# Kernel optimization log

Measured on AMD Instinct MI355X. Metric: run time of the kernel, lower is better.

## Reference

```python
import jax, jax.numpy as jnp
import numpy as np

T, B, D, H, NQ = 2048, 512, 128, 128, 8

def setup_inputs() -> dict:
    key = jax.random.key(0)
    ks = jax.random.split(key, 9)
    s = 1.0 / np.sqrt(D + H)
    inp = {"inputs": jax.random.normal(ks[0], (T, B, D), dtype=jnp.float32)}
    names = ["Wf", "bf", "Wi", "bi", "Wu", "bu", "Wo", "bo"]
    for j, nm in enumerate(names):
        shp = (NQ, D + H) if nm.startswith("W") else (NQ,)
        inp[nm] = jax.random.normal(ks[j + 1], shp, dtype=jnp.float32) * s
    return inp


def _qgate(z):
    # Expected fraction of '1' outcomes after RX(theta_i)|0> on each wire:
    # P(1) = sin^2(theta/2); mean over wires -> one scalar per sample.
    # (Deterministic expectation in place of the 100-shot Aer sampling; the
    # appended random_circuit is unseeded/non-deterministic and is omitted.)
    return jnp.mean(jnp.sin(z * 0.5) ** 2, axis=-1)  # [B]


def reference(inputs, Wf, bf, Wi, bi, Wu, bu, Wo, bo):
    Bsz = inputs.shape[1]
    h0 = jnp.zeros((Bsz, H), dtype=inputs.dtype)
    c0 = jnp.zeros((Bsz, H), dtype=inputs.dtype)

    def step(carry, x):
        hx, cx = carry
        comb = jnp.concatenate([x, hx], axis=1)  # [B, D+H]
        f = jax.nn.sigmoid(_qgate(comb @ Wf.T + bf))[:, None]
        i = jax.nn.sigmoid(_qgate(comb @ Wi.T + bi))[:, None]
        g = jnp.tanh(_qgate(comb @ Wu.T + bu))[:, None]
        o = jax.nn.sigmoid(_qgate(comb @ Wo.T + bo))[:, None]
        cx = f * cx + i * g
        hx = o * jnp.tanh(cx)
        return (hx, cx), hx

    (hx, cx), stacked = jax.lax.scan(step, (h0, c0), inputs)
    return stacked, hx, cx
```

## Files before the change

kernel.cpp:

```cpp
#include <hip/hip_runtime.h>
#include <stdint.h>


typedef __attribute__((ext_vector_type(8))) short short8;
typedef __attribute__((ext_vector_type(4))) float float4v;

#define TSTEPS 2048
#define BATCH  512
#define DIMX   128
#define HID    128
#define TBLK   (TSTEPS / 8)
#define LROW   33
#define LBUF   (16 * LROW)

template <int CTRL>
__device__ __forceinline__ float dppf(float x) {
  return __int_as_float(
      __builtin_amdgcn_mov_dpp(__float_as_int(x), CTRL, 0xF, 0xF, true));
}

__device__ __forceinline__ void splitv(float4v a, float4v b,
                                       short8& hi, short8& lo) {
#pragma unroll
  for (int j = 0; j < 8; ++j) {
    float x = (j < 4) ? a[j] : b[j - 4];
    unsigned int u = __float_as_uint(x);
    float r = x - __uint_as_float(u & 0xFFFF0000u);
    hi[j] = (short)(u >> 16);
    lo[j] = (short)(__float_as_uint(r) >> 16);
  }
}

__global__ __launch_bounds__(64) void qlstm_fused(
    const float* __restrict__ X,
    const float* __restrict__ Wf, const float* __restrict__ bfv,
    const float* __restrict__ Wi, const float* __restrict__ biv,
    const float* __restrict__ Wu, const float* __restrict__ buv,
    const float* __restrict__ Wo, const float* __restrict__ bov,
    float* __restrict__ out)
{
  __shared__ float Zl[2 * LBUF];

  const int lane  = threadIdx.x;
  const int m     = lane & 15;
  const int quad  = lane >> 4;
  const int g32   = lane & 31;
  const int gate  = g32 >> 3;
  const int q     = g32 & 7;
  const int bhalf = lane >> 5;
  const int b0    = blockIdx.x * 2;

  const int qm = m & 7;
  const float* Bt0 = (m < 8) ? Wf : Wi;
  const float* Bt1 = (m < 8) ? Wu : Wo;
  short8 b0h[4], b0l[4], b1h[4], b1l[4];
#pragma unroll
  for (int ks = 0; ks < 4; ++ks) {
    const float* p0 = Bt0 + qm * 256 + ks * 32 + quad * 8;
    const float* p1 = Bt1 + qm * 256 + ks * 32 + quad * 8;
    splitv(*(const float4v*)p0, *(const float4v*)(p0 + 4), b0h[ks], b0l[ks]);
    splitv(*(const float4v*)p1, *(const float4v*)(p1 + 4), b1h[ks], b1l[ks]);
  }
  const float INV2PI = 0.15915494309189535f;
  const float bias0 = ((m < 8) ? bfv : biv)[qm];
  const float bias1 = ((m < 8) ? buv : bov)[qm];

  const float* Wsel = (gate == 0) ? Wf : (gate == 1) ? Wi
                    : (gate == 2) ? Wu : Wo;
  const float* wp = Wsel + q * 256 + 128;
  float ws = 0.f;
#pragma unroll 8
  for (int j = 0; j < 128; ++j) ws += wp[j];
  const float wrev = ws * INV2PI;

  const float L2E = 1.4426950408889634f;
  const float ka = (gate == 2) ? (L2E / 8.f) : (L2E / 16.f);
  const float kb = (gate == 2) ? (-L2E)      : (-0.5f * L2E);
  const float s2 = (gate == 2) ? 2.f : 1.f;
  const float s3 = (gate == 2) ? -1.f : 0.f;

  const int base32 = lane & 32;
  const int adr_f = (base32 + 0  + q) * 4;
  const int adr_i = (base32 + 8  + q) * 4;
  const int adr_u = (base32 + 16 + q) * 4;
  const int adr_o = (base32 + 24 + q) * 4;

  const float* arow = X + ((long)(m >> 1) * BATCH + b0 + (m & 1)) * DIMX;
  float4v Aa[8];

#define LOADA(tb)                                                            \
  {                                                                          \
    const float* p_ = arow + (long)(tb) * (8 * BATCH * DIMX);                \
    _Pragma("unroll")                                                        \
    for (int ks_ = 0; ks_ < 4; ++ks_) {                                      \
      Aa[2 * ks_]     = *(const float4v*)(p_ + ks_ * 32 + quad * 8);         \
      Aa[2 * ks_ + 1] = *(const float4v*)(p_ + ks_ * 32 + quad * 8 + 4);     \
    }                                                                        \
  }

#define PRODUCE(buf)                                                         \
  {                                                                          \
    float4v acc0 = {0.f, 0.f, 0.f, 0.f};                                     \
    float4v acc1 = {0.f, 0.f, 0.f, 0.f};                                     \
    _Pragma("unroll")                                                        \
    for (int ks_ = 0; ks_ < 4; ++ks_) {                                      \
      short8 ah_, al_;                                                       \
      splitv(Aa[2 * ks_], Aa[2 * ks_ + 1], ah_, al_);                        \
      acc0 = __builtin_amdgcn_mfma_f32_16x16x32_bf16(ah_, b0h[ks_], acc0, 0, 0, 0); \
      acc0 = __builtin_amdgcn_mfma_f32_16x16x32_bf16(al_, b0h[ks_], acc0, 0, 0, 0); \
      acc0 = __builtin_amdgcn_mfma_f32_16x16x32_bf16(ah_, b0l[ks_], acc0, 0, 0, 0); \
      acc1 = __builtin_amdgcn_mfma_f32_16x16x32_bf16(ah_, b1h[ks_], acc1, 0, 0, 0); \
      acc1 = __builtin_amdgcn_mfma_f32_16x16x32_bf16(al_, b1h[ks_], acc1, 0, 0, 0); \
      acc1 = __builtin_amdgcn_mfma_f32_16x16x32_bf16(ah_, b1l[ks_], acc1, 0, 0, 0); \
    }                                                                        \
    _Pragma("unroll")                                                        \
    for (int r_ = 0; r_ < 4; ++r_) {                                         \
      int row_ = quad * 4 + r_;                                              \
      Zl[(buf) * LBUF + row_ * LROW + m]      = (acc0[r_] + bias0) * INV2PI; \
      Zl[(buf) * LBUF + row_ * LROW + m + 16] = (acc1[r_] + bias1) * INV2PI; \
    }                                                                        \
  }

  float c = 0.f, h = 0.f;
  float* orow = out + (long)(b0 + bhalf) * HID + g32 * 4;

  LOADA(0);
  PRODUCE(0);
  LOADA(1);

  for (int k = 0; k < TBLK; ++k) {
    PRODUCE((k + 1) & 1);
    int kn = k + 2; if (kn > TBLK - 1) kn = TBLK - 1;
    LOADA(kn);

    const float* zb = Zl + (k & 1) * LBUF + bhalf * LROW + g32;
#pragma unroll
    for (int j = 0; j < 8; ++j) {
      float zx = zb[j * 2 * LROW];

      float r  = __builtin_fmaf(h, wrev, zx);
      float cs = __builtin_amdgcn_cosf(r);

      float s = cs + dppf<0x141>(cs);
      s += dppf<0xB1>(s);
      s += dppf<0x4E>(s);

      float e = __builtin_amdgcn_exp2f(__builtin_fmaf(s, ka, kb));
      float v = __builtin_fmaf(__builtin_amdgcn_rcpf(1.f + e), s2, s3);

      float fg = __int_as_float(__builtin_amdgcn_ds_bpermute(adr_f, __float_as_int(v)));
      float ig = __int_as_float(__builtin_amdgcn_ds_bpermute(adr_i, __float_as_int(v)));
      float ug = __int_as_float(__builtin_amdgcn_ds_bpermute(adr_u, __float_as_int(v)));
      float og = __int_as_float(__builtin_amdgcn_ds_bpermute(adr_o, __float_as_int(v)));

      c = __builtin_fmaf(fg, c, ig * ug);
      float e2 = __builtin_amdgcn_exp2f(c * (2.f * L2E));
      float th = __builtin_fmaf(-2.f, __builtin_amdgcn_rcpf(1.f + e2), 1.f);
      h = og * th;

      float4v hv = {h, h, h, h};
      *(float4v*)orow = hv;
      orow += (long)BATCH * HID;
    }
  }

  float4v hv = {h, h, h, h};
  float4v cv = {c, c, c, c};
  float* hxp = out + (long)TSTEPS * BATCH * HID + (long)(b0 + bhalf) * HID + g32 * 4;
  *(float4v*)hxp = hv;
  *(float4v*)(hxp + BATCH * HID) = cv;
#undef LOADA
#undef PRODUCE
}

extern "C" void kernel_launch(void* const* d_in, const int* in_sizes, int n_in,
                              void* d_out, int out_size, void* d_ws, size_t ws_size,
                              hipStream_t stream) {
  (void)in_sizes; (void)n_in; (void)out_size; (void)d_ws; (void)ws_size;
  const float* X   = (const float*)d_in[0];
  const float* Wf  = (const float*)d_in[1];
  const float* bfv = (const float*)d_in[2];
  const float* Wi  = (const float*)d_in[3];
  const float* biv = (const float*)d_in[4];
  const float* Wu  = (const float*)d_in[5];
  const float* buv = (const float*)d_in[6];
  const float* Wo  = (const float*)d_in[7];
  const float* bov = (const float*)d_in[8];
  float* out = (float*)d_out;

  qlstm_fused<<<BATCH / 2, 64, 0, stream>>>(X, Wf, bfv, Wi, biv, Wu, buv, Wo, bov, out);
}
```

Before: 994.6 us.

## Interleave MFMA production with recurrence and remap lanes to cut cross-lane shuffles

The lane layout changes so that each lane handles two qubits of one gate. Gate values are then broadcast within a quad using DPP instead of four ds_bpermute ops, and the qubit reduction drops from three DPP steps to two. The next block's MFMA work and A-load are spread across the eight serial recurrence steps so the matrix unit overlaps the latency-bound gate chain. The recurrence is also reformulated algebraically: c is tracked in scaled exp2 units, h-dependent terms are precomputed from og and rc, and the ug*2-1 step is folded in. This shortens the dependency chain but changes rounding and adds register pressure.

```diff
diff --git a/kernel.cpp b/kernel.cpp
--- a/kernel.cpp
+++ b/kernel.cpp
@@ -45,8 +45,8 @@
   const int m     = lane & 15;
   const int quad  = lane >> 4;
   const int g32   = lane & 31;
-  const int gate  = g32 >> 3;
-  const int q     = g32 & 7;
+  const int gate  = g32 & 3;
+  const int qq    = (g32 >> 2) & 3;
   const int bhalf = lane >> 5;
   const int b0    = blockIdx.x * 2;
 
@@ -67,23 +67,19 @@
 
   const float* Wsel = (gate == 0) ? Wf : (gate == 1) ? Wi
                     : (gate == 2) ? Wu : Wo;
-  const float* wp = Wsel + q * 256 + 128;
-  float ws = 0.f;
+  const float* wpa = Wsel + qq * 256 + 128;
+  const float* wpb = Wsel + (qq + 4) * 256 + 128;
+  float wsa = 0.f, wsb = 0.f;
 #pragma unroll 8
-  for (int j = 0; j < 128; ++j) ws += wp[j];
-  const float wrev = ws * INV2PI;
+  for (int j = 0; j < 128; ++j) { wsa += wpa[j]; wsb += wpb[j]; }
+  const float wrev0 = wsa * INV2PI;
+  const float wrev1 = wsb * INV2PI;
 
   const float L2E = 1.4426950408889634f;
   const float ka = (gate == 2) ? (L2E / 8.f) : (L2E / 16.f);
   const float kb = (gate == 2) ? (-L2E)      : (-0.5f * L2E);
-  const float s2 = (gate == 2) ? 2.f : 1.f;
-  const float s3 = (gate == 2) ? -1.f : 0.f;
-
-  const int base32 = lane & 32;
-  const int adr_f = (base32 + 0  + q) * 4;
-  const int adr_i = (base32 + 8  + q) * 4;
-  const int adr_u = (base32 + 16 + q) * 4;
-  const int adr_o = (base32 + 24 + q) * 4;
+  const int zc0 = gate * 8 + qq;
+  const int zc1 = zc0 + 4;
 
   const float* arow = X + ((long)(m >> 1) * BATCH + b0 + (m & 1)) * DIMX;
   float4v Aa[8];
@@ -121,7 +117,12 @@
     }                                                                        \
   }
 
-  float c = 0.f, h = 0.f;
+  float cc = 0.f;
+  float rc = 0.f;
+  float og = 0.f;
+  float ogw0 = 0.f, ogw1 = 0.f;
+  float n2g0 = 0.f, n2g1 = 0.f;
+  float h = 0.f;
   float* orow = out + (long)(b0 + bhalf) * HID + g32 * 4;
 
   LOADA(0);
@@ -129,34 +130,70 @@
   LOADA(1);
 
   for (int k = 0; k < TBLK; ++k) {
-    PRODUCE((k + 1) & 1);
-    int kn = k + 2; if (kn > TBLK - 1) kn = TBLK - 1;
-    LOADA(kn);
-
-    const float* zb = Zl + (k & 1) * LBUF + bhalf * LROW + g32;
+    const int wbuf = (k + 1) & 1;
+
+    const float* zb = Zl + (k & 1) * LBUF + bhalf * LROW;
+    float zx0[8], zx1[8];
 #pragma unroll
     for (int j = 0; j < 8; ++j) {
-      float zx = zb[j * 2 * LROW];
-
-      float r  = __builtin_fmaf(h, wrev, zx);
-      float cs = __builtin_amdgcn_cosf(r);
-
-      float s = cs + dppf<0x141>(cs);
-      s += dppf<0xB1>(s);
-      s += dppf<0x4E>(s);
-
-      float e = __builtin_amdgcn_exp2f(__builtin_fmaf(s, ka, kb));
-      float v = __builtin_fmaf(__builtin_amdgcn_rcpf(1.f + e), s2, s3);
-
-      float fg = __int_as_float(__builtin_amdgcn_ds_bpermute(adr_f, __float_as_int(v)));
-      float ig = __int_as_float(__builtin_amdgcn_ds_bpermute(adr_i, __float_as_int(v)));
-      float ug = __int_as_float(__builtin_amdgcn_ds_bpermute(adr_u, __float_as_int(v)));
-      float og = __int_as_float(__builtin_amdgcn_ds_bpermute(adr_o, __float_as_int(v)));
-
-      c = __builtin_fmaf(fg, c, ig * ug);
-      float e2 = __builtin_amdgcn_exp2f(c * (2.f * L2E));
-      float th = __builtin_fmaf(-2.f, __builtin_amdgcn_rcpf(1.f + e2), 1.f);
-      h = og * th;
+      zx0[j] = zb[j * 2 * LROW + zc0];
+      zx1[j] = zb[j * 2 * LROW + zc1];
+    }
+
+    float4v acc0 = {0.f, 0.f, 0.f, 0.f};
+    float4v acc1 = {0.f, 0.f, 0.f, 0.f};
+    short8 ah, al;
+
+#pragma unroll
+    for (int j = 0; j < 8; ++j) {
+      {
+        const int ks = j >> 1;
+        if ((j & 1) == 0) {
+          splitv(Aa[2 * ks], Aa[2 * ks + 1], ah, al);
+          acc0 = __builtin_amdgcn_mfma_f32_16x16x32_bf16(ah, b0h[ks], acc0, 0, 0, 0);
+          acc0 = __builtin_amdgcn_mfma_f32_16x16x32_bf16(al, b0h[ks], acc0, 0, 0, 0);
+          acc0 = __builtin_amdgcn_mfma_f32_16x16x32_bf16(ah, b0l[ks], acc0, 0, 0, 0);
+        } else {
+          acc1 = __builtin_amdgcn_mfma_f32_16x16x32_bf16(ah, b1h[ks], acc1, 0, 0, 0);
+          acc1 = __builtin_amdgcn_mfma_f32_16x16x32_bf16(al, b1h[ks], acc1, 0, 0, 0);
+          acc1 = __builtin_amdgcn_mfma_f32_16x16x32_bf16(ah, b1l[ks], acc1, 0, 0, 0);
+        }
+        if (j == 7) {
+#pragma unroll
+          for (int r_ = 0; r_ < 4; ++r_) {
+            int row_ = quad * 4 + r_;
+            Zl[wbuf * LBUF + row_ * LROW + m]      = (acc0[r_] + bias0) * INV2PI;
+            Zl[wbuf * LBUF + row_ * LROW + m + 16] = (acc1[r_] + bias1) * INV2PI;
+          }
+          int kn = k + 2; if (kn > TBLK - 1) kn = TBLK - 1;
+          LOADA(kn);
+        }
+      }
+
+      float r0 = __builtin_fmaf(n2g0, rc, ogw0 + zx0[j]);
+      float r1 = __builtin_fmaf(n2g1, rc, ogw1 + zx1[j]);
+      float cs = __builtin_amdgcn_cosf(r0) + __builtin_amdgcn_cosf(r1);
+
+      float s1 = cs + dppf<0x124>(cs);
+      float s  = s1 + dppf<0x128>(s1);
+
+      float e  = __builtin_amdgcn_exp2f(__builtin_fmaf(s, ka, kb));
+      float v  = __builtin_amdgcn_rcpf(1.f + e);
+
+      float fg = dppf<0x00>(v);
+      float ig = dppf<0x55>(v);
+      float ug = dppf<0xAA>(v);
+      og       = dppf<0xFF>(v);
+
+      float igug2 = __builtin_fmaf(ug * (4.f * L2E), ig, ig * (-2.f * L2E));
+      cc = __builtin_fmaf(fg, cc, igug2);
+
+      float e2 = __builtin_amdgcn_exp2f(cc);
+      rc = __builtin_amdgcn_rcpf(1.f + e2);
+
+      h = __builtin_fmaf(-2.f * og, rc, og);
+      ogw0 = og * wrev0;  n2g0 = -2.f * ogw0;
+      ogw1 = og * wrev1;  n2g1 = -2.f * ogw1;
 
       float4v hv = {h, h, h, h};
       *(float4v*)orow = hv;
@@ -164,8 +201,10 @@
     }
   }
 
+  const float HALF_LN2 = 0.34657359027997264f;
+  float cfin = cc * HALF_LN2;
   float4v hv = {h, h, h, h};
-  float4v cv = {c, c, c, c};
+  float4v cv = {cfin, cfin, cfin, cfin};
   float* hxp = out + (long)TSTEPS * BATCH * HID + (long)(b0 + bhalf) * HID + g32 * 4;
   *(float4v*)hxp = hv;
   *(float4v*)(hxp + BATCH * HID) = cv;
```

After: 1.082 ms. 1.09x slower.
